# Performance work log

Hardware: AMD Instinct MI355X
Metric: run time of the kernel (lower is better)

The kernel has to match this reference:

```python
import jax, jax.numpy as jnp
import numpy as np

D_MODEL = 1024
NUM_HEADS = 16
HEAD_SIZE = D_MODEL // NUM_HEADS
THETA = 10000.0
MAX_SEQ_LEN = 4096


def _rope_tables():
    # (max_seq_len, head_size//2) cos/sin tables, matching RotaryPositionalEmbedding
    k = jnp.arange(HEAD_SIZE // 2, dtype=jnp.float32)
    inv_freq = 1.0 / (THETA ** (2.0 * k / HEAD_SIZE))
    pos = jnp.arange(MAX_SEQ_LEN, dtype=jnp.float32)
    ang = pos[:, None] * inv_freq[None, :]
    return jnp.cos(ang), jnp.sin(ang)


def _apply_rope(x, cos, sin):
    # x: (b, h, s, d); cos/sin: (s, d//2) -> broadcast over (b, h)
    x1 = x[..., ::2]
    x2 = x[..., 1::2]
    out_even = x1 * cos - x2 * sin
    out_odd = x2 * cos + x1 * sin
    # re-interleave pairs back to (..., d)
    return jnp.stack([out_even, out_odd], axis=-1).reshape(x.shape)


def setup_inputs() -> dict:
    key = jax.random.key(0)
    k1, k2, k3 = jax.random.split(key, 3)
    b, s = 1, 4096
    std_qkv = np.sqrt(2.0 / (D_MODEL + 3 * D_MODEL))
    std_o = np.sqrt(2.0 / (D_MODEL + D_MODEL))
    return {
        "x": jax.random.normal(k1, (b, s, D_MODEL), dtype=jnp.float32),
        "token_positions": jnp.arange(s, dtype=jnp.int32),
        "W_qkv": jax.random.normal(k2, (3 * D_MODEL, D_MODEL), dtype=jnp.float32) * std_qkv,
        "W_o": jax.random.normal(k3, (D_MODEL, D_MODEL), dtype=jnp.float32) * std_o,
    }


def reference(x, token_positions, W_qkv, W_o):
    b, s, _ = x.shape
    qkv = jnp.einsum("bsd,ed->bse", x, W_qkv)  # (b, s, 3*d_model)
    q, k, v = jnp.split(qkv, 3, axis=-1)

    def to_heads(t):
        return t.reshape(b, s, NUM_HEADS, HEAD_SIZE).transpose(0, 2, 1, 3)  # (b, h, s, hs)

    q, k, v = to_heads(q), to_heads(k), to_heads(v)

    cos_tab, sin_tab = _rope_tables()
    cos = cos_tab[token_positions]  # (s, hs//2)
    sin = sin_tab[token_positions]
    q = _apply_rope(q, cos, sin)
    k = _apply_rope(k, cos, sin)

    scale = 1.0 / jnp.sqrt(jnp.asarray(HEAD_SIZE, dtype=x.dtype))
    scores = jnp.einsum("bhqd,bhkd->bhqk", q, k) * scale  # (b, h, s, s)
    causal = jnp.tril(jnp.ones((s, s), dtype=bool))
    scores = jnp.where(causal, scores, jnp.finfo(scores.dtype).min)
    attn = jax.nn.softmax(scores, axis=-1)
    out = jnp.einsum("bhqk,bhkd->bhqd", attn, v)  # (b, h, s, hs)
    out = out.transpose(0, 2, 1, 3).reshape(b, s, D_MODEL)
    return jnp.einsum("bsd,ed->bse", out, W_o)
```

## Files before the change

### kernel.cpp

```cpp
#include <hip/hip_runtime.h>
#include <stdint.h>

typedef unsigned short u16;
typedef __attribute__((ext_vector_type(8))) short bf16x8;
typedef __attribute__((ext_vector_type(4))) float f32x4;

#define LN_THETA 9.210340371976184f
#define SLEN 4096
#define DMODEL 1024

__device__ __forceinline__ u16 f2bf(float f) {
  union { float f; unsigned u; } v; v.f = f;
  unsigned u = v.u;
  return (u16)((u + 0x7FFFu + ((u >> 16) & 1u)) >> 16);
}
__device__ __forceinline__ u16 f2bf_trunc(float f) {
  union { float f; unsigned u; } v; v.f = f;
  return (u16)(v.u >> 16);
}

__device__ __forceinline__ f32x4 mfma16(bf16x8 a, bf16x8 b, f32x4 c) {
  return __builtin_amdgcn_mfma_f32_16x16x32_bf16(a, b, c, 0, 0, 0);
}

__device__ __forceinline__ void async16(const u16* g, u16* l) {
  __builtin_amdgcn_global_load_lds(
      (const __attribute__((address_space(1))) unsigned int*)g,
      (__attribute__((address_space(3))) unsigned int*)l, 16, 0, 0);
}

__global__ void rope_tab_kernel(const int* __restrict__ tokpos,
                                float2* __restrict__ tab) {
  int t = blockIdx.x * 256 + threadIdx.x;
  int s = t >> 5, i = t & 31;
  float inv = expf(-(float)(2 * i) * (LN_THETA / 64.0f));
  float ang = (float)tokpos[s] * inv;
  float sn, cs;
  sincosf(ang, &sn, &cs);
  tab[t] = make_float2(cs, sn);
}

__global__ void cvt_kernel(const float* __restrict__ src, u16* __restrict__ dst,
                           int n4) {
  int i = blockIdx.x * 256 + threadIdx.x;
  if (i >= n4) return;
  float4 v = ((const float4*)src)[i];
  ushort4 o;
  o.x = f2bf(v.x); o.y = f2bf(v.y); o.z = f2bf(v.z); o.w = f2bf(v.w);
  ((ushort4*)dst)[i] = o;
}

__global__ __launch_bounds__(256) void gemm_qkv_kernel(
    const u16* __restrict__ A, const u16* __restrict__ B,
    u16* __restrict__ qb, u16* __restrict__ kb,
    u16* __restrict__ vbT, const float2* __restrict__ cstab) {
  const int K = 1024;
  __shared__ __align__(16) u16 As[128][32];
  __shared__ __align__(16) u16 Bs[128][32];
  const int tid = threadIdx.x;
  const int wave = tid >> 6, lane = tid & 63;
  const int quad = lane >> 4, col = lane & 15;
  const int rowBase = blockIdx.x * 128;
  const int colBase = blockIdx.y * 128;
  const int wm = (wave >> 1) * 64, wn = (wave & 1) * 64;

  const int sRow = wave * 32 + (lane >> 2);
  const int sK = (lane & 3) * 8;
  const u16* gA = A + (size_t)(rowBase + sRow) * K + sK;
  const u16* gB = B + (size_t)(colBase + sRow) * K + sK;

  f32x4 acc[4][4];
#pragma unroll
  for (int i = 0; i < 4; ++i)
#pragma unroll
    for (int j = 0; j < 4; ++j)
      acc[i][j] = f32x4{0.f, 0.f, 0.f, 0.f};

  for (int kk = 0; kk < K; kk += 32) {
    __syncthreads();
    async16(gA + kk, &As[sRow][sK]);
    async16(gA + kk + 16 * K, &As[sRow + 16][sK]);
    async16(gB + kk, &Bs[sRow][sK]);
    async16(gB + kk + 16 * K, &Bs[sRow + 16][sK]);
    __syncthreads();
    bf16x8 af[4], bfr[4];
#pragma unroll
    for (int i = 0; i < 4; ++i)
      af[i] = *(const bf16x8*)&As[wm + i * 16 + col][quad * 8];
#pragma unroll
    for (int j = 0; j < 4; ++j)
      bfr[j] = *(const bf16x8*)&Bs[wn + j * 16 + col][quad * 8];
#pragma unroll
    for (int i = 0; i < 4; ++i)
#pragma unroll
      for (int j = 0; j < 4; ++j)
        acc[i][j] = mfma16(af[i], bfr[j], acc[i][j]);
  }

#pragma unroll
  for (int j = 0; j < 4; ++j) {
    int s = colBase + wn + j * 16 + col;
#pragma unroll
    for (int i = 0; i < 4; ++i) {
      int e0 = rowBase + wm + i * 16 + quad * 4;
      int sec = e0 >> 10;
      int eh = e0 & 1023;
      int hh = eh >> 6, d = eh & 63;
      float v0 = acc[i][j][0], v1 = acc[i][j][1];
      float v2 = acc[i][j][2], v3 = acc[i][j][3];
      if (sec < 2) {
        float2 cs0 = cstab[s * 32 + (d >> 1)];
        float2 cs1 = cstab[s * 32 + (d >> 1) + 1];
        float r0 = v0 * cs0.x - v1 * cs0.y;
        float r1 = v1 * cs0.x + v0 * cs0.y;
        float r2 = v2 * cs1.x - v3 * cs1.y;
        float r3 = v3 * cs1.x + v2 * cs1.y;
        u16* dst = (sec == 0 ? qb : kb) + ((size_t)hh * SLEN + s) * 64 + d;
        dst[0] = f2bf(r0); dst[1] = f2bf(r1);
        dst[2] = f2bf(r2); dst[3] = f2bf(r3);
      } else {
        u16* dst = vbT + ((size_t)hh * 64 + d) * SLEN + s;
        dst[0] = f2bf(v0);
        dst[SLEN] = f2bf(v1);
        dst[2 * SLEN] = f2bf(v2);
        dst[3 * SLEN] = f2bf(v3);
      }
    }
  }
}

__global__ __launch_bounds__(256) void gemm_out_kernel(
    const u16* __restrict__ A, const u16* __restrict__ B,
    float* __restrict__ outf) {
  const int K = 1024;
  __shared__ __align__(16) u16 As[128][32];
  __shared__ __align__(16) u16 Bs[64][32];
  const int tid = threadIdx.x;
  const int wave = tid >> 6, lane = tid & 63;
  const int quad = lane >> 4, col = lane & 15;
  const int rowBase = blockIdx.x * 128;
  const int colBase = blockIdx.y * 64;

  const int sRow = wave * 32 + (lane >> 2);
  const int bRow = wave * 16 + (lane >> 2);
  const int sK = (lane & 3) * 8;
  const u16* gA = A + (size_t)(rowBase + sRow) * K + sK;
  const u16* gB = B + (size_t)(colBase + bRow) * K + sK;

  f32x4 acc[2][4];
#pragma unroll
  for (int i = 0; i < 2; ++i)
#pragma unroll
    for (int j = 0; j < 4; ++j)
      acc[i][j] = f32x4{0.f, 0.f, 0.f, 0.f};

  for (int kk = 0; kk < K; kk += 32) {
    __syncthreads();
    async16(gA + kk, &As[sRow][sK]);
    async16(gA + kk + 16 * K, &As[sRow + 16][sK]);
    async16(gB + kk, &Bs[bRow][sK]);
    __syncthreads();
    bf16x8 af[2], bfr[4];
#pragma unroll
    for (int i = 0; i < 2; ++i)
      af[i] = *(const bf16x8*)&As[wave * 32 + i * 16 + col][quad * 8];
#pragma unroll
    for (int j = 0; j < 4; ++j)
      bfr[j] = *(const bf16x8*)&Bs[j * 16 + col][quad * 8];
#pragma unroll
    for (int i = 0; i < 2; ++i)
#pragma unroll
      for (int j = 0; j < 4; ++j)
        acc[i][j] = mfma16(af[i], bfr[j], acc[i][j]);
  }

#pragma unroll
  for (int i = 0; i < 2; ++i) {
    int r0 = rowBase + wave * 32 + i * 16 + quad * 4;
#pragma unroll
    for (int j = 0; j < 4; ++j) {
      int cc = colBase + j * 16 + col;
#pragma unroll
      for (int r = 0; r < 4; ++r)
        outf[(size_t)(r0 + r) * DMODEL + cc] = acc[i][j][r];
    }
  }
}

__global__ __launch_bounds__(128) void flash_kernel(
    const u16* __restrict__ qbuf, const u16* __restrict__ kbuf,
    const u16* __restrict__ vbT, u16* __restrict__ attn) {
  const int S = SLEN;
  const int h = blockIdx.x;
  const int tile = 63 - (int)blockIdx.y;
  const int wave = threadIdx.x >> 6, lane = threadIdx.x & 63;
  const int quad = lane >> 4, col = lane & 15;
  const u16* Q = qbuf + (size_t)h * S * 64;
  const u16* Kh = kbuf + (size_t)h * S * 64;
  const u16* Vt = vbT + (size_t)h * 64 * S;

  __shared__ __align__(16) u16 Ks[2][64][64];
  __shared__ __align__(16) u16 Vs[2][64][64];
  __shared__ __align__(16) u16 Pld[2][2][16][72];

  const int sr = lane >> 3;
  const int sw = ((lane & 7) ^ sr) * 8;
  const int dcol = (lane & 7) * 8;

  const int segA = ((quad ^ (col & 7)) * 8);
  const int segB = (((quad ^ 4) ^ (col & 7)) * 8);

  const int nch = tile + 1;
  const int qrow0 = tile * 64 + wave * 32;

  bf16x8 qf0[2], qf1[2];
#pragma unroll
  for (int i = 0; i < 2; ++i) {
    const u16* qp = &Q[(size_t)(qrow0 + i * 16 + col) * 64 + quad * 8];
    qf0[i] = *(const bf16x8*)qp;
    qf1[i] = *(const bf16x8*)(qp + 32);
  }

  f32x4 o[2][4];
#pragma unroll
  for (int i = 0; i < 2; ++i)
#pragma unroll
    for (int n = 0; n < 4; ++n) o[i][n] = f32x4{0.f, 0.f, 0.f, 0.f};
  float lrow[2][4] = {{0.f, 0.f, 0.f, 0.f}, {0.f, 0.f, 0.f, 0.f}};

  auto stage = [&](int c, int b) {
    const int k0 = c * 64;
#pragma unroll
    for (int t = 0; t < 4; ++t) {
      int row = (t * 2 + wave) * 8 + sr;
      async16(Kh + (size_t)(k0 + row) * 64 + sw, &Ks[b][row][dcol]);
      async16(Vt + (size_t)row * S + k0 + sw, &Vs[b][row][dcol]);
    }
  };

  stage(0, 0);

  for (int c = 0; c < nch; ++c) {
    const int b = c & 1;
    __syncthreads();
    if (c + 1 < nch) stage(c + 1, b ^ 1);

    bf16x8 kf0[4], kf1[4], vf0[4], vf1[4];
#pragma unroll
    for (int j = 0; j < 4; ++j) {
      kf0[j] = *(const bf16x8*)&Ks[b][16 * j + col][segA];
      kf1[j] = *(const bf16x8*)&Ks[b][16 * j + col][segB];
    }
#pragma unroll
    for (int n = 0; n < 4; ++n) {
      vf0[n] = *(const bf16x8*)&Vs[b][16 * n + col][segA];
      vf1[n] = *(const bf16x8*)&Vs[b][16 * n + col][segB];
    }
    const bool lastc = (c == nch - 1);
#pragma unroll
    for (int i = 0; i < 2; ++i) {
      f32x4 s[4];
#pragma unroll
      for (int j = 0; j < 4; ++j)
        s[j] = mfma16(qf1[i], kf1[j],
                      mfma16(qf0[i], kf0[j], f32x4{0.f, 0.f, 0.f, 0.f}));
      float p[4][4];
#pragma unroll
      for (int r = 0; r < 4; ++r) {
        const int qrel = wave * 32 + i * 16 + quad * 4 + r;
#pragma unroll
        for (int j = 0; j < 4; ++j) {
          float e = __expf(s[j][r] * 0.125f);
          if (lastc && (16 * j + col > qrel)) e = 0.f;
          p[j][r] = e;
        }
        lrow[i][r] += (p[0][r] + p[1][r]) + (p[2][r] + p[3][r]);
      }
#pragma unroll
      for (int j = 0; j < 4; ++j)
#pragma unroll
        for (int r = 0; r < 4; ++r)
          Pld[wave][i][quad * 4 + r][16 * j + col] = f2bf_trunc(p[j][r]);
      bf16x8 pa0 = *(const bf16x8*)&Pld[wave][i][col][quad * 8];
      bf16x8 pa1 = *(const bf16x8*)&Pld[wave][i][col][quad * 8 + 32];
#pragma unroll
      for (int n = 0; n < 4; ++n)
        o[i][n] = mfma16(pa1, vf1[n], mfma16(pa0, vf0[n], o[i][n]));
    }
  }

#pragma unroll
  for (int i = 0; i < 2; ++i) {
#pragma unroll
    for (int m = 1; m <= 8; m <<= 1)
#pragma unroll
      for (int r = 0; r < 4; ++r) lrow[i][r] += __shfl_xor(lrow[i][r], m);
#pragma unroll
    for (int r = 0; r < 4; ++r) {
      float inv = 1.0f / lrow[i][r];
      int row = qrow0 + i * 16 + quad * 4 + r;
      u16* dst = &attn[(size_t)row * DMODEL + h * 64 + col];
#pragma unroll
      for (int n = 0; n < 4; ++n) dst[16 * n] = f2bf(o[i][n][r] * inv);
    }
  }
}

extern "C" void kernel_launch(void* const* d_in, const int* in_sizes, int n_in,
                              void* d_out, int out_size, void* d_ws,
                              size_t ws_size, hipStream_t stream) {
  const float* x = (const float*)d_in[0];
  const int* tokpos = (const int*)d_in[1];
  const float* wqkv = (const float*)d_in[2];
  const float* wo = (const float*)d_in[3];
  float* out = (float*)d_out;

  char* ws = (char*)d_ws;
  u16* xb    = (u16*)(ws);
  u16* wqkvb = (u16*)(ws + ((size_t)8 << 20));
  u16* wob   = (u16*)(ws + ((size_t)14 << 20));
  u16* qb    = (u16*)(ws + ((size_t)16 << 20));
  u16* kb    = (u16*)(ws + ((size_t)24 << 20));
  u16* vbT   = (u16*)(ws + ((size_t)32 << 20));
  u16* attn  = (u16*)(ws + ((size_t)40 << 20));
  float2* cstab = (float2*)(ws + ((size_t)48 << 20));

  rope_tab_kernel<<<dim3(512), dim3(256), 0, stream>>>(tokpos, cstab);
  cvt_kernel<<<dim3(4096), dim3(256), 0, stream>>>(x, xb, 1 << 20);
  cvt_kernel<<<dim3(3072), dim3(256), 0, stream>>>(wqkv, wqkvb, 3 << 18);
  cvt_kernel<<<dim3(1024), dim3(256), 0, stream>>>(wo, wob, 1 << 18);
  gemm_qkv_kernel<<<dim3(24, 32), dim3(256), 0, stream>>>(
      wqkvb, xb, qb, kb, vbT, cstab);
  flash_kernel<<<dim3(16, 64), dim3(128), 0, stream>>>(qb, kb, vbT, attn);
  gemm_out_kernel<<<dim3(32, 16), dim3(256), 0, stream>>>(attn, wob, out);
}
```

Before: 253.9 us.

## Stage QKV epilogue through LDS and enlarge flash query tiles to 128 rows

The QKV GEMM epilogue now writes rotated Q/K and transposed V into a shared-memory tile, then stores contiguous 16-byte vectors to global memory. This replaces the scattered 2-byte writes, especially the strided V-transpose stores. The flash kernel moves to 4 waves covering 128 query rows per block, so each staged K/V chunk is reused by twice as many rows. Blocks are ordered to interleave long and short tiles, with per-subtile skipping and masking. The trade-offs are extra LDS (a 34KB staging buffer) and fewer, larger flash blocks.

```diff
diff --git a/kernel.cpp b/kernel.cpp
--- a/kernel.cpp
+++ b/kernel.cpp
@@ -57,6 +57,7 @@
   const int K = 1024;
   __shared__ __align__(16) u16 As[128][32];
   __shared__ __align__(16) u16 Bs[128][32];
+  __shared__ __align__(16) u16 Ts[128][136];
   const int tid = threadIdx.x;
   const int wave = tid >> 6, lane = tid & 63;
   const int quad = lane >> 4, col = lane & 15;
@@ -97,35 +98,58 @@
         acc[i][j] = mfma16(af[i], bfr[j], acc[i][j]);
   }
 
-#pragma unroll
-  for (int j = 0; j < 4; ++j) {
-    int s = colBase + wn + j * 16 + col;
-#pragma unroll
-    for (int i = 0; i < 4; ++i) {
-      int e0 = rowBase + wm + i * 16 + quad * 4;
-      int sec = e0 >> 10;
-      int eh = e0 & 1023;
-      int hh = eh >> 6, d = eh & 63;
-      float v0 = acc[i][j][0], v1 = acc[i][j][1];
-      float v2 = acc[i][j][2], v3 = acc[i][j][3];
-      if (sec < 2) {
+  const int sec = rowBase >> 10;
+
+  if (sec < 2) {
+#pragma unroll
+    for (int j = 0; j < 4; ++j) {
+      int sl = wn + j * 16 + col;
+      int s = colBase + sl;
+#pragma unroll
+      for (int i = 0; i < 4; ++i) {
+        int el = wm + i * 16 + quad * 4;
+        int d = (rowBase + el) & 63;
+        float v0 = acc[i][j][0], v1 = acc[i][j][1];
+        float v2 = acc[i][j][2], v3 = acc[i][j][3];
         float2 cs0 = cstab[s * 32 + (d >> 1)];
         float2 cs1 = cstab[s * 32 + (d >> 1) + 1];
-        float r0 = v0 * cs0.x - v1 * cs0.y;
-        float r1 = v1 * cs0.x + v0 * cs0.y;
-        float r2 = v2 * cs1.x - v3 * cs1.y;
-        float r3 = v3 * cs1.x + v2 * cs1.y;
-        u16* dst = (sec == 0 ? qb : kb) + ((size_t)hh * SLEN + s) * 64 + d;
-        dst[0] = f2bf(r0); dst[1] = f2bf(r1);
-        dst[2] = f2bf(r2); dst[3] = f2bf(r3);
-      } else {
-        u16* dst = vbT + ((size_t)hh * 64 + d) * SLEN + s;
-        dst[0] = f2bf(v0);
-        dst[SLEN] = f2bf(v1);
-        dst[2 * SLEN] = f2bf(v2);
-        dst[3 * SLEN] = f2bf(v3);
+        ushort4 pk;
+        pk.x = f2bf(v0 * cs0.x - v1 * cs0.y);
+        pk.y = f2bf(v1 * cs0.x + v0 * cs0.y);
+        pk.z = f2bf(v2 * cs1.x - v3 * cs1.y);
+        pk.w = f2bf(v3 * cs1.x + v2 * cs1.y);
+        *(ushort4*)&Ts[sl][el] = pk;
       }
     }
+    __syncthreads();
+    int sl = tid >> 1, hf = tid & 1;
+    int hh = ((rowBase & 1023) >> 6) + hf;
+    u16* dst = (sec == 0 ? qb : kb) + ((size_t)hh * SLEN + colBase + sl) * 64;
+    const u16* srcp = &Ts[sl][hf * 64];
+#pragma unroll
+    for (int kq = 0; kq < 8; ++kq)
+      ((int4*)dst)[kq] = ((const int4*)srcp)[kq];
+  } else {
+#pragma unroll
+    for (int j = 0; j < 4; ++j) {
+      int sl = wn + j * 16 + col;
+#pragma unroll
+      for (int i = 0; i < 4; ++i) {
+        int el = wm + i * 16 + quad * 4;
+#pragma unroll
+        for (int r = 0; r < 4; ++r)
+          Ts[el + r][sl] = f2bf(acc[i][j][r]);
+      }
+    }
+    __syncthreads();
+    int el = tid >> 1, sh = tid & 1;
+    int e = rowBase - 2048 + el;
+    int hh = e >> 6, d = e & 63;
+    u16* dst = vbT + (size_t)(hh * 64 + d) * SLEN + colBase + sh * 64;
+    const u16* srcp = &Ts[el][sh * 64];
+#pragma unroll
+    for (int kq = 0; kq < 8; ++kq)
+      ((int4*)dst)[kq] = ((const int4*)srcp)[kq];
   }
 }
 
@@ -187,12 +211,13 @@
   }
 }
 
-__global__ __launch_bounds__(128) void flash_kernel(
+__global__ __launch_bounds__(256) void flash_kernel(
     const u16* __restrict__ qbuf, const u16* __restrict__ kbuf,
     const u16* __restrict__ vbT, u16* __restrict__ attn) {
   const int S = SLEN;
   const int h = blockIdx.x;
-  const int tile = 63 - (int)blockIdx.y;
+  const int yy = blockIdx.y;
+  const int tile = (yy < 16) ? (31 - yy) : (yy - 16);
   const int wave = threadIdx.x >> 6, lane = threadIdx.x & 63;
   const int quad = lane >> 4, col = lane & 15;
   const u16* Q = qbuf + (size_t)h * S * 64;
@@ -201,17 +226,16 @@
 
   __shared__ __align__(16) u16 Ks[2][64][64];
   __shared__ __align__(16) u16 Vs[2][64][64];
-  __shared__ __align__(16) u16 Pld[2][2][16][72];
+  __shared__ __align__(16) u16 Pld[4][2][16][72];
 
   const int sr = lane >> 3;
   const int sw = ((lane & 7) ^ sr) * 8;
   const int dcol = (lane & 7) * 8;
-
   const int segA = ((quad ^ (col & 7)) * 8);
   const int segB = (((quad ^ 4) ^ (col & 7)) * 8);
 
-  const int nch = tile + 1;
-  const int qrow0 = tile * 64 + wave * 32;
+  const int nch = 2 * tile + 2;
+  const int qrow0 = tile * 128 + wave * 32;
 
   bf16x8 qf0[2], qf1[2];
 #pragma unroll
@@ -231,8 +255,8 @@
   auto stage = [&](int c, int b) {
     const int k0 = c * 64;
 #pragma unroll
-    for (int t = 0; t < 4; ++t) {
-      int row = (t * 2 + wave) * 8 + sr;
+    for (int t = 0; t < 2; ++t) {
+      int row = (t * 4 + wave) * 8 + sr;
       async16(Kh + (size_t)(k0 + row) * 64 + sw, &Ks[b][row][dcol]);
       async16(Vt + (size_t)row * S + k0 + sw, &Vs[b][row][dcol]);
     }
@@ -242,6 +266,7 @@
 
   for (int c = 0; c < nch; ++c) {
     const int b = c & 1;
+    const int k0 = c * 64;
     __syncthreads();
     if (c + 1 < nch) stage(c + 1, b ^ 1);
 
@@ -256,9 +281,11 @@
       vf0[n] = *(const bf16x8*)&Vs[b][16 * n + col][segA];
       vf1[n] = *(const bf16x8*)&Vs[b][16 * n + col][segB];
     }
-    const bool lastc = (c == nch - 1);
 #pragma unroll
     for (int i = 0; i < 2; ++i) {
+      const int qs0 = qrow0 + i * 16;
+      if (k0 > qs0 + 15) continue;
+      const bool needmask = (k0 + 63 > qs0);
       f32x4 s[4];
 #pragma unroll
       for (int j = 0; j < 4; ++j)
@@ -267,11 +294,11 @@
       float p[4][4];
 #pragma unroll
       for (int r = 0; r < 4; ++r) {
-        const int qrel = wave * 32 + i * 16 + quad * 4 + r;
+        const int qabs = qs0 + quad * 4 + r;
 #pragma unroll
         for (int j = 0; j < 4; ++j) {
           float e = __expf(s[j][r] * 0.125f);
-          if (lastc && (16 * j + col > qrel)) e = 0.f;
+          if (needmask && (k0 + 16 * j + col > qabs)) e = 0.f;
           p[j][r] = e;
         }
         lrow[i][r] += (p[0][r] + p[1][r]) + (p[2][r] + p[3][r]);
@@ -331,6 +358,6 @@
   cvt_kernel<<<dim3(1024), dim3(256), 0, stream>>>(wo, wob, 1 << 18);
   gemm_qkv_kernel<<<dim3(24, 32), dim3(256), 0, stream>>>(
       wqkvb, xb, qb, kb, vbT, cstab);
-  flash_kernel<<<dim3(16, 64), dim3(128), 0, stream>>>(qb, kb, vbT, attn);
+  flash_kernel<<<dim3(16, 32), dim3(256), 0, stream>>>(qb, kb, vbT, attn);
   gemm_out_kernel<<<dim3(32, 16), dim3(256), 0, stream>>>(attn, wob, out);
 }
```

Result: slower. 273.0 us (+7.5%).
